# Kernel optimization log

Measured on AMD Instinct MI355X. Metric: run time of the kernel, lower is better.

## Reference

```python
import jax, jax.numpy as jnp
import numpy as np

T, B, I, H = 512, 64, 1024, 1024
DROPOUT = 0.3


def setup_inputs() -> dict:
    key = jax.random.key(0)
    k = jax.random.split(key, 6)
    s = 1.0 / np.sqrt(H).astype(np.float32)
    x = jax.random.normal(k[0], (T, B, I), dtype=jnp.float32)
    w_ih = jax.random.uniform(k[1], (4 * H, I), minval=-s, maxval=s, dtype=jnp.float32)
    w_hh = jax.random.uniform(k[2], (4 * H, H), minval=-s, maxval=s, dtype=jnp.float32)
    b_ih = jax.random.uniform(k[3], (4 * H,), minval=-s, maxval=s, dtype=jnp.float32)
    b_hh = jax.random.uniform(k[4], (4 * H,), minval=-s, maxval=s, dtype=jnp.float32)
    # init_weights: forget-gate bias (second quarter) set to 1
    b_ih = b_ih.at[H:2 * H].set(1.0)
    b_hh = b_hh.at[H:2 * H].set(1.0)
    # DropConnect mask on recurrent weights (training-mode dropout, fixed realization)
    keep = jax.random.bernoulli(k[5], 1.0 - DROPOUT, (4 * H, H))
    hh_mask = keep.astype(jnp.float32) / (1.0 - DROPOUT)
    return {"x": x, "w_ih": w_ih, "w_hh": w_hh, "b_ih": b_ih, "b_hh": b_hh, "hh_mask": hh_mask}


def reference(x, w_ih, w_hh, b_ih, b_hh, hh_mask):
    # x: (T, B, I). PyTorch LSTM gate order: i, f, g, o.
    h = w_hh.shape[1]
    w_hh_dropped = w_hh * hh_mask  # DropConnect applied once per forward
    # Precompute input contribution for all timesteps (one big GEMM): (T, B, 4H)
    gx = jnp.einsum('tbi,gi->tbg', x, w_ih) + b_ih + b_hh

    def step(carry, g_t):
        h_t, c_t = carry
        gates = g_t + h_t @ w_hh_dropped.T  # (B, 4H)
        i_g, f_g, g_g, o_g = jnp.split(gates, 4, axis=-1)
        i_g = jax.nn.sigmoid(i_g)
        f_g = jax.nn.sigmoid(f_g)
        g_g = jnp.tanh(g_g)
        o_g = jax.nn.sigmoid(o_g)
        c_new = f_g * c_t + i_g * g_g
        h_new = o_g * jnp.tanh(c_new)
        return (h_new, c_new), h_new

    bsz = x.shape[1]
    init = (jnp.zeros((bsz, h), x.dtype), jnp.zeros((bsz, h), x.dtype))
    (hn, cn), out = jax.lax.scan(step, init, gx)
    # match torch: output (T,B,H), hn/cn with leading num_layers dim
    return out, hn[None], cn[None]
```

## Files before the change

kernel.cpp:

```cpp
#include <hip/hip_runtime.h>

#define TT 512
#define BB 64
#define II 1024
#define HH 1024
#define GG 4096
#define BH 65536
#define NBLK 128

typedef __attribute__((ext_vector_type(8))) short bf16x8;
typedef __attribute__((ext_vector_type(4))) float f32x4;

__device__ __forceinline__ float bf2f(unsigned short u) {
  union { unsigned int i; float f; } v; v.i = ((unsigned int)u) << 16; return v.f;
}
__device__ __forceinline__ unsigned short f2bf(float f) {
  union { float f; unsigned int i; } v; v.f = f;
  return (unsigned short)((v.i + 0x7FFFu + ((v.i >> 16) & 1u)) >> 16);
}
__device__ __forceinline__ bf16x8 pack8(float4 a, float4 b) {
  union { bf16x8 v; unsigned short u[8]; } p;
  p.u[0] = f2bf(a.x); p.u[1] = f2bf(a.y); p.u[2] = f2bf(a.z); p.u[3] = f2bf(a.w);
  p.u[4] = f2bf(b.x); p.u[5] = f2bf(b.y); p.u[6] = f2bf(b.z); p.u[7] = f2bf(b.w);
  return p.v;
}
__device__ __forceinline__ float sigmoid_f(float x) { return 1.0f / (1.0f + __expf(-x)); }
__device__ __forceinline__ float tanh_f(float x) {
  float e = __expf(-2.0f * fabsf(x));
  float t = (1.0f - e) / (1.0f + e);
  return copysignf(t, x);
}

__device__ __forceinline__ void st32_uc(unsigned* p, unsigned v) {
  __hip_atomic_store(p, v, __ATOMIC_RELAXED, __HIP_MEMORY_SCOPE_AGENT);
}
__device__ __forceinline__ unsigned ld32_uc(const unsigned* p) {
  return __hip_atomic_load(p, __ATOMIC_RELAXED, __HIP_MEMORY_SCOPE_AGENT);
}

__device__ __forceinline__ void wait_flags(const unsigned* flags, int t) {
  if (threadIdx.x < 64) {
    const unsigned* f0 = flags + (2 * threadIdx.x) * 16;
    const unsigned* f1 = flags + (2 * threadIdx.x + 1) * 16;
    while ((int)ld32_uc(f0) < t || (int)ld32_uc(f1) < t)
      __builtin_amdgcn_s_sleep(1);
  }
  __syncthreads();
}

__global__ __launch_bounds__(256) void wdlstm_gemm_gx(
    const float* __restrict__ xc, const float* __restrict__ w_ih,
    const float* __restrict__ b_ih, const float* __restrict__ b_hh,
    unsigned short* __restrict__ gxc) {
  __shared__ __align__(16) char As[16384];
  __shared__ __align__(16) char Bs[16384];

  const int tid = threadIdx.x;
  const int bx  = blockIdx.x;
  const int tm  = bx >> 5, tn = bx & 31;
  const int m0  = tm * 128, n0 = tn * 128;
  const int wv  = tid >> 6, l = tid & 63;
  const int wr  = wv >> 1, wc = wv & 1;
  const int ln  = l & 15, lq = l >> 4;

  f32x4 acc[4][4];
#pragma unroll
  for (int i = 0; i < 4; ++i)
#pragma unroll
    for (int j = 0; j < 4; ++j) acc[i][j] = (f32x4){0.f, 0.f, 0.f, 0.f};

  for (int kt = 0; kt < 16; ++kt) {
    const int k0 = kt * 64;
    __syncthreads();
#pragma unroll
    for (int o = 0; o < 4; ++o) {
      int c2 = tid + 256 * o;
      int row = c2 >> 3, q8 = c2 & 7;
      int addr = (row * 128 + q8 * 16) ^ ((row & 7) << 4);
      {
        const float* s = xc + (size_t)(m0 + row) * II + k0 + q8 * 8;
        float4 a0 = *(const float4*)s;
        float4 a1 = *(const float4*)(s + 4);
        *(bf16x8*)(As + addr) = pack8(a0, a1);
      }
      {
        const float* s = w_ih + (size_t)(n0 + row) * II + k0 + q8 * 8;
        float4 a0 = *(const float4*)s;
        float4 a1 = *(const float4*)(s + 4);
        *(bf16x8*)(Bs + addr) = pack8(a0, a1);
      }
    }
    __syncthreads();
#pragma unroll
    for (int kc = 0; kc < 2; ++kc) {
      bf16x8 af[4], bfr[4];
#pragma unroll
      for (int mi = 0; mi < 4; ++mi) {
        int row = 64 * wr + 16 * mi + ln;
        int addr = (row * 128 + kc * 64 + lq * 16) ^ ((row & 7) << 4);
        af[mi] = *(const bf16x8*)(As + addr);
      }
#pragma unroll
      for (int ni = 0; ni < 4; ++ni) {
        int row = 64 * wc + 16 * ni + ln;
        int addr = (row * 128 + kc * 64 + lq * 16) ^ ((row & 7) << 4);
        bfr[ni] = *(const bf16x8*)(Bs + addr);
      }
#pragma unroll
      for (int mi = 0; mi < 4; ++mi)
#pragma unroll
        for (int ni = 0; ni < 4; ++ni)
          acc[mi][ni] = __builtin_amdgcn_mfma_f32_16x16x32_bf16(af[mi], bfr[ni], acc[mi][ni], 0, 0, 0);
    }
  }
#pragma unroll
  for (int mi = 0; mi < 4; ++mi)
#pragma unroll
    for (int ni = 0; ni < 4; ++ni) {
      int col = n0 + 64 * wc + 16 * ni + ln;
      float bv = b_ih[col] + b_hh[col];
#pragma unroll
      for (int r = 0; r < 4; ++r) {
        int row = m0 + 64 * wr + 16 * mi + 4 * lq + r;
        gxc[(size_t)row * GG + col] = f2bf(acc[mi][ni][r] + bv);
      }
    }
}

__global__ __launch_bounds__(256) void wdlstm_recurrence(
    const float* __restrict__ w_hh, const float* __restrict__ hh_mask,
    const unsigned short* __restrict__ gxc,
    float* __restrict__ out, float* __restrict__ c_state,
    unsigned* __restrict__ flags,
    unsigned short* __restrict__ hinit,
    unsigned short* __restrict__ hring,
    int t0, int tc) {
  __shared__ __align__(16) char Wlds[65536];
  __shared__ float Dlds[64][35];

  const int tid = threadIdx.x;
  const int wv  = tid >> 6, l = tid & 63;
  const int ln  = l & 15, lq = l >> 4;
  const int j0h = blockIdx.x * 8;

#pragma unroll
  for (int c8 = 0; c8 < 16; ++c8) {
    int c = tid + 256 * c8;
    int n = c >> 7, cc = c & 127;
    int wrow = (n >> 3) * HH + j0h + (n & 7);
    const float* sw = w_hh   + (size_t)wrow * HH + cc * 8;
    const float* sm = hh_mask + (size_t)wrow * HH + cc * 8;
    float4 w0 = *(const float4*)sw, w1 = *(const float4*)(sw + 4);
    float4 m0 = *(const float4*)sm, m1 = *(const float4*)(sm + 4);
    float4 p0 = {w0.x * m0.x, w0.y * m0.y, w0.z * m0.z, w0.w * m0.w};
    float4 p1 = {w1.x * m1.x, w1.y * m1.y, w1.z * m1.z, w1.w * m1.w};
    int addr = (n * 2048 + cc * 16) ^ ((n & 7) << 4);
    *(bf16x8*)(Wlds + addr) = pack8(p0, p1);
  }
  __syncthreads();

  const int b_ep = l;
  const int jj0  = 2 * wv;
  float c_reg[2];
  if (t0 == 0) {
    c_reg[0] = c_reg[1] = 0.f;
  } else {
    float2 cv = *(const float2*)(c_state + (size_t)b_ep * HH + j0h + jj0);
    c_reg[0] = cv.x; c_reg[1] = cv.y;
  }

  float* hn_out = out + (size_t)TT * BH;
  float* cn_out = hn_out + BH;

  float gxv[4][2];
#pragma unroll
  for (int g = 0; g < 4; ++g) {
    unsigned u = *(const unsigned*)(gxc + (size_t)b_ep * GG + g * HH + j0h + jj0);
    gxv[g][0] = bf2f((unsigned short)u);
    gxv[g][1] = bf2f((unsigned short)(u >> 16));
  }

  for (int lt = 0; lt < tc; ++lt) {
    const int t = t0 + lt;

    f32x4 acc[2];
    acc[0] = (f32x4){0.f, 0.f, 0.f, 0.f};
    acc[1] = (f32x4){0.f, 0.f, 0.f, 0.f};

    if (t > 0) {
      wait_flags(flags, t);
      const unsigned short* hp = (lt == 0) ? hinit
                                           : hring + (size_t)(lt - 1) * BH;
      const unsigned short* ap = hp + (size_t)(16 * wv + ln) * HH + lq * 8;
#pragma unroll 4
      for (int kc = 0; kc < 32; ++kc) {
        bf16x8 a = *(const bf16x8*)(ap + kc * 32);
#pragma unroll
        for (int ni = 0; ni < 2; ++ni) {
          int n = 16 * ni + ln;
          int baddr = (n * 2048 + kc * 64 + lq * 16) ^ ((n & 7) << 4);
          bf16x8 b = *(const bf16x8*)(Wlds + baddr);
          acc[ni] = __builtin_amdgcn_mfma_f32_16x16x32_bf16(a, b, acc[ni], 0, 0, 0);
        }
      }
    }
#pragma unroll
    for (int ni = 0; ni < 2; ++ni)
#pragma unroll
      for (int r = 0; r < 4; ++r)
        Dlds[16 * wv + 4 * lq + r][16 * ni + ln] = acc[ni][r];
    __syncthreads();

    float hq[2];
#pragma unroll
    for (int q = 0; q < 2; ++q) {
      float g0 = Dlds[b_ep][ 0 + jj0 + q] + gxv[0][q];
      float g1 = Dlds[b_ep][ 8 + jj0 + q] + gxv[1][q];
      float g2 = Dlds[b_ep][16 + jj0 + q] + gxv[2][q];
      float g3 = Dlds[b_ep][24 + jj0 + q] + gxv[3][q];
      float ig = sigmoid_f(g0);
      float fg = sigmoid_f(g1);
      float gg = tanh_f(g2);
      float og = sigmoid_f(g3);
      c_reg[q] = fg * c_reg[q] + ig * gg;
      hq[q] = og * tanh_f(c_reg[q]);
    }
    *(float2*)(out + (size_t)t * BH + (size_t)b_ep * HH + j0h + jj0) = make_float2(hq[0], hq[1]);
    unsigned hpack = (unsigned)f2bf(hq[0]) | ((unsigned)f2bf(hq[1]) << 16);
    unsigned* hr32 = (unsigned*)(hring + (size_t)lt * BH);
    st32_uc(hr32 + (((size_t)b_ep * HH + j0h + jj0) >> 1), hpack);
    if (lt == tc - 1) {
      unsigned* hi32 = (unsigned*)hinit;
      st32_uc(hi32 + (((size_t)b_ep * HH + j0h + jj0) >> 1), hpack);
    }
    if (t == TT - 1) {
      *(float2*)(hn_out + (size_t)b_ep * HH + j0h + jj0) = make_float2(hq[0], hq[1]);
      *(float2*)(cn_out + (size_t)b_ep * HH + j0h + jj0) = make_float2(c_reg[0], c_reg[1]);
    }

    if (lt + 1 < tc) {
#pragma unroll
      for (int g = 0; g < 4; ++g) {
        unsigned u = *(const unsigned*)(gxc + ((size_t)(lt + 1) * BB + b_ep) * GG + g * HH + j0h + jj0);
        gxv[g][0] = bf2f((unsigned short)u);
        gxv[g][1] = bf2f((unsigned short)(u >> 16));
      }
    }

    __syncthreads();
    if (tid == 0) st32_uc(&flags[blockIdx.x * 16], (unsigned)(t + 1));
  }

  *(float2*)(c_state + (size_t)b_ep * HH + j0h + jj0) = make_float2(c_reg[0], c_reg[1]);
}

extern "C" void kernel_launch(void* const* d_in, const int* in_sizes, int n_in,
                              void* d_out, int out_size, void* d_ws, size_t ws_size,
                              hipStream_t stream) {
  const float* x       = (const float*)d_in[0];
  const float* w_ih    = (const float*)d_in[1];
  const float* w_hh    = (const float*)d_in[2];
  const float* b_ih    = (const float*)d_in[3];
  const float* b_hh    = (const float*)d_in[4];
  const float* hh_mask = (const float*)d_in[5];
  float* out           = (float*)d_out;

  char* ws = (char*)d_ws;
  float* c_state        = (float*)ws;
  unsigned* flags       = (unsigned*)(ws + 262144);
  unsigned short* hinit = (unsigned short*)(ws + 278528);
  unsigned short* hring = (unsigned short*)(ws + 409600);

  const long long fixed = 409600;
  const long long per_t = 524288 + 131072;
  long long avail = (long long)ws_size - fixed;
  int TC = (int)(avail / per_t);
  if (TC > 128) TC = 128;
  TC &= ~1;
  if (TC < 2) TC = 2;
  unsigned short* gxc = (unsigned short*)(ws + 409600 + (size_t)TC * 131072);

  hipMemsetAsync(flags, 0, 16384, stream);

  for (int t0 = 0; t0 < TT; t0 += TC) {
    int tc = TT - t0 < TC ? TT - t0 : TC;
    const float* xc = x + (size_t)t0 * BB * II;
    int grid = (tc * 64 / 128) * 32;
    wdlstm_gemm_gx<<<grid, 256, 0, stream>>>(xc, w_ih, b_ih, b_hh, gxc);
    wdlstm_recurrence<<<NBLK, 256, 0, stream>>>(w_hh, hh_mask, gxc, out, c_state,
                                                flags, hinit, hring, t0, tc);
  }
}
```

Measured before the change: 4.663 ms.

## Centralize step barrier via block 0 and pack h stores into 128-bit writes

```diff
diff --git a/kernel.cpp b/kernel.cpp
--- a/kernel.cpp
+++ b/kernel.cpp
@@ -10,6 +10,7 @@
 
 typedef __attribute__((ext_vector_type(8))) short bf16x8;
 typedef __attribute__((ext_vector_type(4))) float f32x4;
+typedef __attribute__((ext_vector_type(4))) unsigned u32x4;
 
 __device__ __forceinline__ float bf2f(unsigned short u) {
   union { unsigned int i; float f; } v; v.i = ((unsigned int)u) << 16; return v.f;
@@ -37,15 +38,8 @@
 __device__ __forceinline__ unsigned ld32_uc(const unsigned* p) {
   return __hip_atomic_load(p, __ATOMIC_RELAXED, __HIP_MEMORY_SCOPE_AGENT);
 }
-
-__device__ __forceinline__ void wait_flags(const unsigned* flags, int t) {
-  if (threadIdx.x < 64) {
-    const unsigned* f0 = flags + (2 * threadIdx.x) * 16;
-    const unsigned* f1 = flags + (2 * threadIdx.x + 1) * 16;
-    while ((int)ld32_uc(f0) < t || (int)ld32_uc(f1) < t)
-      __builtin_amdgcn_s_sleep(1);
-  }
-  __syncthreads();
+__device__ __forceinline__ void st128_uc(void* p, u32x4 v) {
+  asm volatile("global_store_dwordx4 %0, %1, off sc0 sc1" :: "v"(p), "v"(v) : "memory");
 }
 
 __global__ __launch_bounds__(256) void wdlstm_gemm_gx(
@@ -137,11 +131,13 @@
     int t0, int tc) {
   __shared__ __align__(16) char Wlds[65536];
   __shared__ float Dlds[64][35];
+  __shared__ __align__(16) unsigned Hs[64][4];
 
   const int tid = threadIdx.x;
   const int wv  = tid >> 6, l = tid & 63;
   const int ln  = l & 15, lq = l >> 4;
   const int j0h = blockIdx.x * 8;
+  unsigned* g_step = flags + 2048;
 
 #pragma unroll
   for (int c8 = 0; c8 < 16; ++c8) {
@@ -188,7 +184,22 @@
     acc[1] = (f32x4){0.f, 0.f, 0.f, 0.f};
 
     if (t > 0) {
-      wait_flags(flags, t);
+      if (blockIdx.x == 0) {
+        if (tid < 64) {
+          const unsigned* f0 = flags + (2 * tid) * 16;
+          const unsigned* f1 = flags + (2 * tid + 1) * 16;
+          while ((int)ld32_uc(f0) < t || (int)ld32_uc(f1) < t)
+            __builtin_amdgcn_s_sleep(1);
+          if (tid == 0) st32_uc(g_step, (unsigned)t);
+        }
+        __syncthreads();
+      } else {
+        if (tid == 0) {
+          while ((int)ld32_uc(g_step) < t) __builtin_amdgcn_s_sleep(1);
+        }
+        __syncthreads();
+      }
+
       const unsigned short* hp = (lt == 0) ? hinit
                                            : hring + (size_t)(lt - 1) * BH;
       const unsigned short* ap = hp + (size_t)(16 * wv + ln) * HH + lq * 8;
@@ -226,13 +237,7 @@
       hq[q] = og * tanh_f(c_reg[q]);
     }
     *(float2*)(out + (size_t)t * BH + (size_t)b_ep * HH + j0h + jj0) = make_float2(hq[0], hq[1]);
-    unsigned hpack = (unsigned)f2bf(hq[0]) | ((unsigned)f2bf(hq[1]) << 16);
-    unsigned* hr32 = (unsigned*)(hring + (size_t)lt * BH);
-    st32_uc(hr32 + (((size_t)b_ep * HH + j0h + jj0) >> 1), hpack);
-    if (lt == tc - 1) {
-      unsigned* hi32 = (unsigned*)hinit;
-      st32_uc(hi32 + (((size_t)b_ep * HH + j0h + jj0) >> 1), hpack);
-    }
+    Hs[b_ep][wv] = (unsigned)f2bf(hq[0]) | ((unsigned)f2bf(hq[1]) << 16);
     if (t == TT - 1) {
       *(float2*)(hn_out + (size_t)b_ep * HH + j0h + jj0) = make_float2(hq[0], hq[1]);
       *(float2*)(cn_out + (size_t)b_ep * HH + j0h + jj0) = make_float2(c_reg[0], c_reg[1]);
@@ -248,7 +253,18 @@
     }
 
     __syncthreads();
-    if (tid == 0) st32_uc(&flags[blockIdx.x * 16], (unsigned)(t + 1));
+
+    if (wv == 0) {
+      u32x4 hv4 = *(const u32x4*)&Hs[l][0];
+      char* dst = (char*)hring + ((size_t)lt * BH + (size_t)l * HH + j0h) * 2;
+      st128_uc(dst, hv4);
+      if (lt == tc - 1) {
+        char* dsti = (char*)hinit + ((size_t)l * HH + j0h) * 2;
+        st128_uc(dsti, hv4);
+      }
+      asm volatile("s_waitcnt vmcnt(0)" ::: "memory");
+      if (tid == 0) st32_uc(&flags[blockIdx.x * 16], (unsigned)(t + 1));
+    }
   }
 
   *(float2*)(c_state + (size_t)b_ep * HH + j0h + jj0) = make_float2(c_reg[0], c_reg[1]);
```

After: 4.539 ms. -2.7%, faster.
